# Optimization experiments

Measured on AMD Instinct MI355X. Metric: run time of the kernel, lower is better.

The kernel has to match this reference:

```python
import jax, jax.numpy as jnp
import numpy as np

EMBED_DIM = 1024
NUM_HEADS = 16
HEAD_DIM = EMBED_DIM // NUM_HEADS


def setup_inputs() -> dict:
    key = jax.random.key(0)
    ks = jax.random.split(key, 11)
    N, S, D = 2, 2048, EMBED_DIM
    scale = 1.0 / np.sqrt(D)
    inp = {
        "query": jax.random.normal(ks[0], (N, S, D), jnp.float32),
        "key": jax.random.normal(ks[1], (N, S, D), jnp.float32),
        "value": jax.random.normal(ks[2], (N, S, D), jnp.float32),
        # Dense layer params (kernel [D_in, D_out], bias [D_out])
        "Wq": jax.random.normal(ks[3], (D, D), jnp.float32) * scale,
        "bq": jnp.zeros((D,), jnp.float32),
        "Wk": jax.random.normal(ks[4], (D, D), jnp.float32) * scale,
        "bk": jnp.zeros((D,), jnp.float32),
        "Wv": jax.random.normal(ks[5], (D, D), jnp.float32) * scale,
        "bv": jnp.zeros((D,), jnp.float32),
        "Wp": jax.random.normal(ks[6], (D, D), jnp.float32) * scale,
        "bp": jnp.zeros((D,), jnp.float32),
    }
    return inp


def reference(query, key, value, Wq, bq, Wk, bk, Wv, bv, Wp, bp):
    N, S, D = query.shape
    H, Hd = NUM_HEADS, D // NUM_HEADS
    # Linear projections, then split heads: [N, H, S, Hd]
    def split_heads(x):
        return x.reshape(N, S, H, Hd).transpose(0, 2, 1, 3)
    q = split_heads(query @ Wq + bq)
    k = split_heads(key @ Wk + bk)
    v = split_heads(value @ Wv + bv)
    # Scaled dot-product attention; materializes [N, H, S, S] scores
    e = jnp.einsum("bhsd,bhtd->bhst", q, k) / jnp.sqrt(jnp.asarray(Hd, jnp.float32))
    a = jax.nn.softmax(e, axis=-1)
    # Dropout is identity in inference mode (keras Dropout default)
    out = jnp.einsum("bhst,bhtd->bhsd", a, v)
    out = out.transpose(0, 2, 1, 3).reshape(N, S, D)
    return out @ Wp + bp
```

## Files before the change

kernel.cpp:

```cpp
#include <hip/hip_runtime.h>
#include <cstdint>
#include <cstddef>

typedef _Float16 f16;
typedef f16 f16x2 __attribute__((ext_vector_type(2)));
typedef f16 f16x8 __attribute__((ext_vector_type(8)));
typedef __fp16 hf16x2 __attribute__((ext_vector_type(2)));
typedef float f32x4 __attribute__((ext_vector_type(4)));
typedef float f32x16 __attribute__((ext_vector_type(16)));
typedef unsigned int u32;

#define S_LEN 2048
#define DIM 1024
#define NBATCH 2
#define NHEAD 16
#define HDIM 64
#define M_TOT (NBATCH * S_LEN)

#define QSCALE 0.18033688011112042f

#define OFF_XQ 0ull
#define OFF_XK (OFF_XQ + (size_t)M_TOT * DIM * 2)
#define OFF_XV (OFF_XK + (size_t)M_TOT * DIM * 2)
#define OFF_WT (OFF_XV + (size_t)M_TOT * DIM * 2)
#define OFF_Q  (OFF_WT + 4ull * DIM * DIM * 2)
#define OFF_K  (OFF_Q + (size_t)M_TOT * DIM * 2)
#define OFF_VT (OFF_K + (size_t)M_TOT * DIM * 2)
#define OFF_AO (OFF_VT + (size_t)M_TOT * DIM * 2)

typedef const __attribute__((address_space(1))) void GVp;
typedef __attribute__((address_space(3))) void LVp;
__device__ __forceinline__ void gload16(const void* g, void* l) {
  __builtin_amdgcn_global_load_lds((GVp*)g, (LVp*)l, 16, 0, 0);
}

__device__ __forceinline__ float fast_exp2(float x) {
  float r;
  asm("v_exp_f32 %0, %1" : "=v"(r) : "v"(x));
  return r;
}

__global__ __launch_bounds__(256) void cast_x_kernel(
    const float* __restrict__ q, const float* __restrict__ k, const float* __restrict__ v,
    f16* __restrict__ oq, f16* __restrict__ ok, f16* __restrict__ ov) {
  const float* src = blockIdx.y == 0 ? q : blockIdx.y == 1 ? k : v;
  f16* dst = blockIdx.y == 0 ? oq : blockIdx.y == 1 ? ok : ov;
  size_t i = ((size_t)blockIdx.x * 256 + threadIdx.x) * 8;
  float4 a = *(const float4*)(src + i);
  float4 b = *(const float4*)(src + i + 4);
  f16x8 o;
  o[0] = (f16)a.x; o[1] = (f16)a.y; o[2] = (f16)a.z; o[3] = (f16)a.w;
  o[4] = (f16)b.x; o[5] = (f16)b.y; o[6] = (f16)b.z; o[7] = (f16)b.w;
  *(f16x8*)(dst + i) = o;
}

__global__ __launch_bounds__(256) void transpose_w_kernel(
    const float* __restrict__ Wq, const float* __restrict__ Wk,
    const float* __restrict__ Wv, const float* __restrict__ Wp,
    f16* __restrict__ out) {
  const float* W = blockIdx.z == 0 ? Wq : blockIdx.z == 1 ? Wk : blockIdx.z == 2 ? Wv : Wp;
  f16* Wt = out + (size_t)blockIdx.z * DIM * DIM;
  __shared__ f16 tile[64][72];
  const int kt = blockIdx.x * 64, nt = blockIdx.y * 64;
  const int t = threadIdx.x, r = t >> 2, c0 = (t & 3) * 16;
#pragma unroll
  for (int i = 0; i < 16; i += 4) {
    float4 vv = *(const float4*)(W + (size_t)(kt + r) * DIM + nt + c0 + i);
    tile[r][c0 + i + 0] = (f16)vv.x; tile[r][c0 + i + 1] = (f16)vv.y;
    tile[r][c0 + i + 2] = (f16)vv.z; tile[r][c0 + i + 3] = (f16)vv.w;
  }
  __syncthreads();
  f16x8 o0, o1;
#pragma unroll
  for (int i = 0; i < 8; ++i) { o0[i] = tile[c0 + i][r]; o1[i] = tile[c0 + 8 + i][r]; }
  *(f16x8*)(Wt + (size_t)(nt + r) * DIM + kt + c0) = o0;
  *(f16x8*)(Wt + (size_t)(nt + r) * DIM + kt + c0 + 8) = o1;
}

__device__ __forceinline__ void gemm_core(const f16* __restrict__ A, const f16* __restrict__ B,
                                          char* lds, f32x4 acc[4][4]) {
  const int tid = threadIdx.x;
  const int wid = tid >> 6, lane = tid & 63;
  const int l15 = lane & 15, l4 = lane >> 4;
  const int wm = (wid >> 1) * 64, wn = (wid & 1) * 64;
  const int srow = tid >> 2;
  const int scol = (tid & 3) * 8;
  const f16* gA = A + (size_t)srow * DIM + scol;
  const f16* gB = B + (size_t)srow * DIM + scol;
  const int ldst = wid * 1024;

  gload16(gA,            lds + ldst);
  gload16(gA + 64 * DIM, lds + 4096 + ldst);
  gload16(gB,            lds + 8192 + ldst);
  gload16(gB + 64 * DIM, lds + 12288 + ldst);
  __syncthreads();

  for (int kt = 0; kt < DIM / 32; ++kt) {
    char* cur = lds + (kt & 1) * 16384;
    if (kt + 1 < DIM / 32) {
      char* nxt = lds + ((kt + 1) & 1) * 16384;
      const f16* ga = gA + (kt + 1) * 32;
      const f16* gb = gB + (kt + 1) * 32;
      gload16(ga,            nxt + ldst);
      gload16(ga + 64 * DIM, nxt + 4096 + ldst);
      gload16(gb,            nxt + 8192 + ldst);
      gload16(gb + 64 * DIM, nxt + 12288 + ldst);
    }
    f16x8 af[4], bf[4];
#pragma unroll
    for (int mt = 0; mt < 4; ++mt)
      af[mt] = *(const f16x8*)(cur + (wm + mt * 16 + l15) * 64 + l4 * 16);
#pragma unroll
    for (int nt = 0; nt < 4; ++nt)
      bf[nt] = *(const f16x8*)(cur + 8192 + (wn + nt * 16 + l15) * 64 + l4 * 16);
#pragma unroll
    for (int mt = 0; mt < 4; ++mt)
#pragma unroll
      for (int nt = 0; nt < 4; ++nt)
        acc[mt][nt] = __builtin_amdgcn_mfma_f32_16x16x32_f16(af[mt], bf[nt], acc[mt][nt], 0, 0, 0);
    __syncthreads();
  }
}


__global__ __launch_bounds__(256) void proj_kernel(
    const f16* __restrict__ Xq, const f16* __restrict__ Xk, const f16* __restrict__ Xv,
    const f16* __restrict__ Wt,
    const float* __restrict__ bq, const float* __restrict__ bk, const float* __restrict__ bv,
    f16* __restrict__ Q, f16* __restrict__ Kh, f16* __restrict__ Vt) {
  __shared__ __align__(16) char lds[32768];
  const int m0 = blockIdx.x * 128, n0 = blockIdx.y * 128;
  const int z = blockIdx.z;
  const f16* X = z == 0 ? Xq : z == 1 ? Xk : Xv;
  const f16* W = Wt + (size_t)z * DIM * DIM;
  const float* bias = z == 0 ? bq : z == 1 ? bk : bv;
  f32x4 acc[4][4] = {};
  gemm_core(X + (size_t)m0 * DIM, W + (size_t)n0 * DIM, lds, acc);

  const int tid = threadIdx.x, wid = tid >> 6, lane = tid & 63;
  const int l15 = lane & 15, l4 = lane >> 4;
  const int wm = (wid >> 1) * 64, wn = (wid & 1) * 64;
#pragma unroll
  for (int nt = 0; nt < 4; ++nt) {
    const int col = n0 + wn + nt * 16 + l15;
    const float bb = bias[col];
    const int hh = col >> 6, d = col & 63;
#pragma unroll
    for (int mt = 0; mt < 4; ++mt)
#pragma unroll
      for (int j = 0; j < 4; ++j) {
        const int row = m0 + wm + mt * 16 + l4 * 4 + j;
        const float v = acc[mt][nt][j] + bb;
        const int n = row >> 11, s = row & (S_LEN - 1);
        const size_t panel = (size_t)(n * NHEAD + hh);
        if (z == 0) {
          const size_t a = panel * (S_LEN * HDIM) + (size_t)(s >> 5) * 2048 +
                           (d >> 4) * 512 + ((d >> 3) & 1) * 256 + (s & 31) * 8 + (d & 7);
          Q[a] = (f16)(v * QSCALE);
        } else if (z == 1) {
          const size_t a = panel * (S_LEN * HDIM) + (size_t)(s >> 5) * 2048 +
                           (d >> 4) * 512 + ((d >> 3) & 1) * 256 + (s & 31) * 8 + (d & 7);
          Kh[a] = (f16)v;
        } else {
          const size_t a = panel * (S_LEN * HDIM) + (size_t)(s >> 6) * 4096 +
                           (d >> 5) * 2048 + ((s >> 4) & 3) * 512 + ((s >> 3) & 1) * 256 +
                           (d & 31) * 8 + (s & 7);
          Vt[a] = (f16)v;
        }
      }
  }
}

__global__ __launch_bounds__(256) void outproj_kernel(
    const f16* __restrict__ A, const f16* __restrict__ Wt,
    const float* __restrict__ bias, float* __restrict__ Out) {
  __shared__ __align__(16) char lds[32768];
  const int m0 = blockIdx.x * 128, n0 = blockIdx.y * 128;
  f32x4 acc[4][4] = {};
  gemm_core(A + (size_t)m0 * DIM, Wt + (size_t)n0 * DIM, lds, acc);

  const int tid = threadIdx.x, wid = tid >> 6, lane = tid & 63;
  const int l15 = lane & 15, l4 = lane >> 4;
  const int wm = (wid >> 1) * 64, wn = (wid & 1) * 64;
#pragma unroll
  for (int nt = 0; nt < 4; ++nt) {
    const int col = n0 + wn + nt * 16 + l15;
    const float bb = bias[col];
#pragma unroll
    for (int mt = 0; mt < 4; ++mt)
#pragma unroll
      for (int j = 0; j < 4; ++j) {
        const int row = m0 + wm + mt * 16 + l4 * 4 + j;
        Out[(size_t)row * DIM + col] = acc[mt][nt][j] + bb;
      }
  }
}

__global__ __launch_bounds__(256, 2) void attn_kernel(
    const f16* __restrict__ Q, const f16* __restrict__ K,
    const f16* __restrict__ Vt, f16* __restrict__ AO) {
  const int qt = blockIdx.x, h = blockIdx.y, b = blockIdx.z;
  const int tid = threadIdx.x;
  const int lane = tid & 63, wid = tid >> 6;
  const int l31 = lane & 31, hi = lane >> 5;

  __shared__ __align__(16) char kv_lds[2][16384];

  const int q0 = qt * 128 + wid * 32;
  const size_t panel = (size_t)(b * NHEAD + h) * (S_LEN * HDIM);
  const f16* Qp = Q + panel + (size_t)(q0 >> 5) * 2048;
  const char* KpB = (const char*)(K + panel);
  const char* VpB = (const char*)(Vt + panel);

  f16x8 qf[4];
#pragma unroll
  for (int sk = 0; sk < 4; ++sk)
    qf[sk] = *(const f16x8*)(Qp + sk * 512 + hi * 256 + l31 * 8);

  f32x16 accO[2] = {};
  float lacc0 = 0.f, lacc1 = 0.f, lacc2 = 0.f, lacc3 = 0.f;

  auto STAGE = [&](int it, int buf) {
    const char* gK = KpB + (size_t)it * 8192 + tid * 16;
    const char* gV = VpB + (size_t)it * 8192 + tid * 16;
    char* lb = kv_lds[buf] + (tid >> 6) * 1024;
    gload16(gK,        lb);
    gload16(gK + 4096, lb + 4096);
    gload16(gV,        lb + 8192);
    gload16(gV + 4096, lb + 12288);
  };

  auto QK = [&](int buf, f32x16 (&st)[2]) {
    const char* lk = kv_lds[buf];
    f16x8 kf[2][4];
#pragma unroll
    for (int tt = 0; tt < 2; ++tt)
#pragma unroll
      for (int sk = 0; sk < 4; ++sk)
        kf[tt][sk] = *(const f16x8*)(lk + tt * 4096 + sk * 1024 + lane * 16);
    __builtin_amdgcn_s_setprio(1);
#pragma unroll
    for (int tt = 0; tt < 2; ++tt) {
      st[tt] = (f32x16)(0.f);
#pragma unroll
      for (int sk = 0; sk < 4; ++sk)
        st[tt] = __builtin_amdgcn_mfma_f32_32x32x16_f16(kf[tt][sk], qf[sk], st[tt], 0, 0, 0);
    }
    __builtin_amdgcn_s_setprio(0);
  };

  auto PHASE = [&](f32x16 (&st)[2], int buf) {
    const char* lv = kv_lds[buf] + 8192;
    f16x8 vf[2][4];
#pragma unroll
    for (int dt = 0; dt < 2; ++dt)
#pragma unroll
      for (int s = 0; s < 4; ++s)
        vf[dt][s] = *(const f16x8*)(lv + dt * 4096 + s * 1024 + lane * 16);

    u32 pk[2][8];
#pragma unroll
    for (int tt = 0; tt < 2; ++tt)
#pragma unroll
      for (int j = 0; j < 8; ++j) {
        const float p0 = fast_exp2(st[tt][2 * j]);
        const float p1 = fast_exp2(st[tt][2 * j + 1]);
        const float ps = p0 + p1;
        if (((tt * 8 + j) & 3) == 0) lacc0 += ps;
        else if (((tt * 8 + j) & 3) == 1) lacc1 += ps;
        else if (((tt * 8 + j) & 3) == 2) lacc2 += ps;
        else lacc3 += ps;
        union { hf16x2 h; u32 w; } cv;
        cv.h = __builtin_amdgcn_cvt_pkrtz(p0, p1);
        pk[tt][j] = cv.w;
      }

    __builtin_amdgcn_s_setprio(1);
#pragma unroll
    for (int s = 0; s < 4; ++s) {
      const int tt = s >> 1, sl = s & 1;
      u32 w0 = pk[tt][4 * sl + 0], w2 = pk[tt][4 * sl + 2];
      u32 w1 = pk[tt][4 * sl + 1], w3 = pk[tt][4 * sl + 3];
      asm("v_permlane32_swap_b32 %0, %1" : "+v"(w0), "+v"(w2));
      asm("v_permlane32_swap_b32 %0, %1" : "+v"(w1), "+v"(w3));
      union { u32 w[4]; f16x8 v; } pf;
      pf.w[0] = w0; pf.w[1] = w1; pf.w[2] = w2; pf.w[3] = w3;
      accO[0] = __builtin_amdgcn_mfma_f32_32x32x16_f16(vf[0][s], pf.v, accO[0], 0, 0, 0);
      accO[1] = __builtin_amdgcn_mfma_f32_32x32x16_f16(vf[1][s], pf.v, accO[1], 0, 0, 0);
    }
    __builtin_amdgcn_s_setprio(0);
  };

  const int NIT = S_LEN / 64;
  STAGE(0, 0);
  __syncthreads();

  f32x16 st[2];
  for (int it = 0; it < NIT; ++it) {
    const int buf = it & 1;
    if (it + 1 < NIT) STAGE(it + 1, buf ^ 1);
    QK(buf, st);
    PHASE(st, buf);
    __syncthreads();
  }

  const float l_loc = (lacc0 + lacc1) + (lacc2 + lacc3);
  const float l_all = l_loc + __shfl_xor(l_loc, 32);
  const float inv = 1.f / l_all;
  f16* aop = AO + ((size_t)(b * S_LEN + q0 + l31)) * DIM + h * HDIM;
#pragma unroll
  for (int dt = 0; dt < 2; ++dt)
#pragma unroll
    for (int j = 0; j < 8; ++j) {
      union { f16x2 h; u32 w; } cv;
      cv.h[0] = (f16)(accO[dt][2 * j] * inv);
      cv.h[1] = (f16)(accO[dt][2 * j + 1] * inv);
      const int d = ((2 * j) & 3) + 8 * ((2 * j) >> 2) + 4 * hi + dt * 32;
      *(f16x2*)(aop + d) = cv.h;
    }
}

extern "C" void kernel_launch(void* const* d_in, const int* in_sizes, int n_in,
                              void* d_out, int out_size, void* d_ws, size_t ws_size,
                              hipStream_t stream) {
  (void)in_sizes; (void)n_in; (void)out_size; (void)ws_size;
  const float* q  = (const float*)d_in[0];
  const float* k  = (const float*)d_in[1];
  const float* v  = (const float*)d_in[2];
  const float* Wq = (const float*)d_in[3];
  const float* bq = (const float*)d_in[4];
  const float* Wk = (const float*)d_in[5];
  const float* bk = (const float*)d_in[6];
  const float* Wv = (const float*)d_in[7];
  const float* bv = (const float*)d_in[8];
  const float* Wp = (const float*)d_in[9];
  const float* bp = (const float*)d_in[10];

  char* ws = (char*)d_ws;
  f16* Xq  = (f16*)(ws + OFF_XQ);
  f16* Xk  = (f16*)(ws + OFF_XK);
  f16* Xv  = (f16*)(ws + OFF_XV);
  f16* Wt  = (f16*)(ws + OFF_WT);
  f16* Qs  = (f16*)(ws + OFF_Q);
  f16* Kh  = (f16*)(ws + OFF_K);
  f16* Vts = (f16*)(ws + OFF_VT);
  f16* AO  = (f16*)(ws + OFF_AO);

  cast_x_kernel<<<dim3(2048, 3, 1), 256, 0, stream>>>(q, k, v, Xq, Xk, Xv);
  transpose_w_kernel<<<dim3(16, 16, 4), 256, 0, stream>>>(Wq, Wk, Wv, Wp, Wt);
  proj_kernel<<<dim3(32, 8, 3), 256, 0, stream>>>(Xq, Xk, Xv, Wt, bq, bk, bv, Qs, Kh, Vts);
  attn_kernel<<<dim3(16, 16, 2), 256, 0, stream>>>(Qs, Kh, Vts, AO);
  outproj_kernel<<<dim3(32, 8, 1), 256, 0, stream>>>(AO, Wt + 3ull * DIM * DIM, bp, (float*)d_out);
}
```

Measured before the change: 131.8 us.

## Split attention KV sequence across two wave groups and merge via LDS

The attention block grows to 512 threads, and two groups of four waves each handle half of the key/value sequence for the same 128 query rows. The partial outputs and row sums are then combined through shared memory before normalisation. This doubles the waves working on each query tile, which is meant to hide latency and keep the same grid of 512 blocks fuller on the GPU. The cost is a larger LDS footprint, an extra barrier and LDS round trip in the epilogue, and launch bounds of one block per 512 threads. Skipping the running max is safe because the combine is a plain sum.

```diff
diff --git a/kernel.cpp b/kernel.cpp
--- a/kernel.cpp
+++ b/kernel.cpp
@@ -196,17 +196,18 @@
   }
 }
 
-__global__ __launch_bounds__(256, 2) void attn_kernel(
+__global__ __launch_bounds__(512, 1) void attn_kernel(
     const f16* __restrict__ Q, const f16* __restrict__ K,
     const f16* __restrict__ Vt, f16* __restrict__ AO) {
   const int qt = blockIdx.x, h = blockIdx.y, b = blockIdx.z;
   const int tid = threadIdx.x;
   const int lane = tid & 63, wid = tid >> 6;
+  const int half = wid >> 2, widh = wid & 3;
   const int l31 = lane & 31, hi = lane >> 5;
 
-  __shared__ __align__(16) char kv_lds[2][16384];
-
-  const int q0 = qt * 128 + wid * 32;
+  __shared__ __align__(16) char kv_lds[2][2][16384];
+
+  const int q0 = qt * 128 + widh * 32;
   const size_t panel = (size_t)(b * NHEAD + h) * (S_LEN * HDIM);
   const f16* Qp = Q + panel + (size_t)(q0 >> 5) * 2048;
   const char* KpB = (const char*)(K + panel);
@@ -220,10 +221,13 @@
   f32x16 accO[2] = {};
   float lacc0 = 0.f, lacc1 = 0.f, lacc2 = 0.f, lacc3 = 0.f;
 
+  const int NIT = S_LEN / 64 / 2;
+
   auto STAGE = [&](int it, int buf) {
-    const char* gK = KpB + (size_t)it * 8192 + tid * 16;
-    const char* gV = VpB + (size_t)it * 8192 + tid * 16;
-    char* lb = kv_lds[buf] + (tid >> 6) * 1024;
+    const int gt = half * NIT + it;
+    const char* gK = KpB + (size_t)gt * 8192 + (widh * 64 + lane) * 16;
+    const char* gV = VpB + (size_t)gt * 8192 + (widh * 64 + lane) * 16;
+    char* lb = &kv_lds[half][buf][widh * 1024];
     gload16(gK,        lb);
     gload16(gK + 4096, lb + 4096);
     gload16(gV,        lb + 8192);
@@ -231,7 +235,7 @@
   };
 
   auto QK = [&](int buf, f32x16 (&st)[2]) {
-    const char* lk = kv_lds[buf];
+    const char* lk = &kv_lds[half][buf][0];
     f16x8 kf[2][4];
 #pragma unroll
     for (int tt = 0; tt < 2; ++tt)
@@ -250,7 +254,7 @@
   };
 
   auto PHASE = [&](f32x16 (&st)[2], int buf) {
-    const char* lv = kv_lds[buf] + 8192;
+    const char* lv = &kv_lds[half][buf][8192];
     f16x8 vf[2][4];
 #pragma unroll
     for (int dt = 0; dt < 2; ++dt)
@@ -291,7 +295,6 @@
     __builtin_amdgcn_s_setprio(0);
   };
 
-  const int NIT = S_LEN / 64;
   STAGE(0, 0);
   __syncthreads();
 
@@ -305,19 +308,39 @@
   }
 
   const float l_loc = (lacc0 + lacc1) + (lacc2 + lacc3);
-  const float l_all = l_loc + __shfl_xor(l_loc, 32);
-  const float inv = 1.f / l_all;
-  f16* aop = AO + ((size_t)(b * S_LEN + q0 + l31)) * DIM + h * HDIM;
-#pragma unroll
-  for (int dt = 0; dt < 2; ++dt)
-#pragma unroll
-    for (int j = 0; j < 8; ++j) {
-      union { f16x2 h; u32 w; } cv;
-      cv.h[0] = (f16)(accO[dt][2 * j] * inv);
-      cv.h[1] = (f16)(accO[dt][2 * j + 1] * inv);
-      const int d = ((2 * j) & 3) + 8 * ((2 * j) >> 2) + 4 * hi + dt * 32;
-      *(f16x2*)(aop + d) = cv.h;
-    }
+  float* comb = (float*)&kv_lds[0][0][0];
+  if (wid >= 4) {
+    float* base = comb + widh * 2048;
+#pragma unroll
+    for (int dt = 0; dt < 2; ++dt)
+#pragma unroll
+      for (int j = 0; j < 16; ++j)
+        base[(dt * 16 + j) * 64 + lane] = accO[dt][j];
+    comb[8192 + widh * 64 + lane] = l_loc;
+  }
+  __syncthreads();
+  if (wid < 4) {
+    float* base = comb + widh * 2048;
+#pragma unroll
+    for (int dt = 0; dt < 2; ++dt)
+#pragma unroll
+      for (int j = 0; j < 16; ++j)
+        accO[dt][j] += base[(dt * 16 + j) * 64 + lane];
+    const float l2 = l_loc + comb[8192 + widh * 64 + lane];
+    const float l_all = l2 + __shfl_xor(l2, 32);
+    const float inv = 1.f / l_all;
+    f16* aop = AO + ((size_t)(b * S_LEN + q0 + l31)) * DIM + h * HDIM;
+#pragma unroll
+    for (int dt = 0; dt < 2; ++dt)
+#pragma unroll
+      for (int j = 0; j < 8; ++j) {
+        union { f16x2 h; u32 w; } cv;
+        cv.h[0] = (f16)(accO[dt][2 * j] * inv);
+        cv.h[1] = (f16)(accO[dt][2 * j + 1] * inv);
+        const int d = ((2 * j) & 3) + 8 * ((2 * j) >> 2) + 4 * hi + dt * 32;
+        *(f16x2*)(aop + d) = cv.h;
+      }
+  }
 }
 
 extern "C" void kernel_launch(void* const* d_in, const int* in_sizes, int n_in,
@@ -349,6 +372,6 @@
   cast_x_kernel<<<dim3(2048, 3, 1), 256, 0, stream>>>(q, k, v, Xq, Xk, Xv);
   transpose_w_kernel<<<dim3(16, 16, 4), 256, 0, stream>>>(Wq, Wk, Wv, Wp, Wt);
   proj_kernel<<<dim3(32, 8, 3), 256, 0, stream>>>(Xq, Xk, Xv, Wt, bq, bk, bv, Qs, Kh, Vts);
-  attn_kernel<<<dim3(16, 16, 2), 256, 0, stream>>>(Qs, Kh, Vts, AO);
+  attn_kernel<<<dim3(16, 16, 2), 512, 0, stream>>>(Qs, Kh, Vts, AO);
   outproj_kernel<<<dim3(32, 8, 1), 256, 0, stream>>>(AO, Wt + 3ull * DIM * DIM, bp, (float*)d_out);
 }
```

Measured after the change: 134.6 us. +2.1%, slower.

## Triple-buffer K/V LDS staging with prefetch distance two in attention

Applied to the files above, without the earlier changes.

The attention loop now uses three LDS buffers instead of two and issues the K/V loads two tiles ahead. The full __syncthreads is replaced by an explicit vmcnt wait plus s_barrier, so only the oldest pending stage must land before compute. The goal is to hide more global-to-LDS latency behind the QK and PV MFMAs. The cost is 48KB of LDS per block instead of 32KB, which may limit occupancy, plus reliance on hand-counted vmcnt values.

```diff
diff --git a/kernel.cpp b/kernel.cpp
--- a/kernel.cpp
+++ b/kernel.cpp
@@ -204,7 +204,7 @@
   const int lane = tid & 63, wid = tid >> 6;
   const int l31 = lane & 31, hi = lane >> 5;
 
-  __shared__ __align__(16) char kv_lds[2][16384];
+  __shared__ __align__(16) char kv_lds[3][16384];
 
   const int q0 = qt * 128 + wid * 32;
   const size_t panel = (size_t)(b * NHEAD + h) * (S_LEN * HDIM);
@@ -223,7 +223,7 @@
   auto STAGE = [&](int it, int buf) {
     const char* gK = KpB + (size_t)it * 8192 + tid * 16;
     const char* gV = VpB + (size_t)it * 8192 + tid * 16;
-    char* lb = kv_lds[buf] + (tid >> 6) * 1024;
+    char* lb = &kv_lds[buf][wid * 1024];
     gload16(gK,        lb);
     gload16(gK + 4096, lb + 4096);
     gload16(gV,        lb + 8192);
@@ -231,7 +231,7 @@
   };
 
   auto QK = [&](int buf, f32x16 (&st)[2]) {
-    const char* lk = kv_lds[buf];
+    const char* lk = &kv_lds[buf][0];
     f16x8 kf[2][4];
 #pragma unroll
     for (int tt = 0; tt < 2; ++tt)
@@ -250,7 +250,7 @@
   };
 
   auto PHASE = [&](f32x16 (&st)[2], int buf) {
-    const char* lv = kv_lds[buf] + 8192;
+    const char* lv = &kv_lds[buf][8192];
     f16x8 vf[2][4];
 #pragma unroll
     for (int dt = 0; dt < 2; ++dt)
@@ -292,17 +292,31 @@
   };
 
   const int NIT = S_LEN / 64;
+
   STAGE(0, 0);
-  __syncthreads();
+  STAGE(1, 1);
 
   f32x16 st[2];
-  for (int it = 0; it < NIT; ++it) {
-    const int buf = it & 1;
-    if (it + 1 < NIT) STAGE(it + 1, buf ^ 1);
-    QK(buf, st);
-    PHASE(st, buf);
-    __syncthreads();
-  }
+  int bcur = 0;
+  for (int it = 0; it < NIT - 1; ++it) {
+    asm volatile("s_waitcnt vmcnt(4)" ::: "memory");
+    __builtin_amdgcn_sched_barrier(0);
+    __builtin_amdgcn_s_barrier();
+    __builtin_amdgcn_sched_barrier(0);
+    if (it + 2 < NIT) {
+      int bn = bcur + 2; if (bn >= 3) bn -= 3;
+      STAGE(it + 2, bn);
+    }
+    QK(bcur, st);
+    PHASE(st, bcur);
+    if (++bcur >= 3) bcur = 0;
+  }
+  asm volatile("s_waitcnt vmcnt(0)" ::: "memory");
+  __builtin_amdgcn_sched_barrier(0);
+  __builtin_amdgcn_s_barrier();
+  __builtin_amdgcn_sched_barrier(0);
+  QK(bcur, st);
+  PHASE(st, bcur);
 
   const float l_loc = (lacc0 + lacc1) + (lacc2 + lacc3);
   const float l_all = l_loc + __shfl_xor(l_loc, 32);
```

New measurement: 132.0 us. About the same (+0.1%).

## Split attention KV range across two blocks, add combine kernel, swizzle GEMM LDS

Applied to the files above, without the earlier changes.

Each attention block now handles only half of the key/value sequence. The grid doubles to 1024 blocks, and the launch bound asks for 4 blocks per CU to improve occupancy. Unnormalized partial outputs and row sums go to workspace (reusing the Xq/Xv cast buffers), and a new combine kernel sums them and normalizes. This works without a max correction because the softmax has no max subtraction. The projection GEMM core also gets an XOR swizzle on LDS columns to reduce bank conflicts. In exchange, the extra kernel launch and the fp16 partial round-trip add memory traffic and some rounding.

```diff
diff --git a/kernel.cpp b/kernel.cpp
--- a/kernel.cpp
+++ b/kernel.cpp
@@ -77,16 +77,16 @@
   *(f16x8*)(Wt + (size_t)(nt + r) * DIM + kt + c0 + 8) = o1;
 }
 
-__device__ __forceinline__ void gemm_core(const f16* __restrict__ A, const f16* __restrict__ B,
-                                          char* lds, f32x4 acc[4][4]) {
+__device__ __forceinline__ void gemm_core_sw(const f16* __restrict__ A, const f16* __restrict__ B,
+                                             char* lds, f32x4 acc[4][4]) {
   const int tid = threadIdx.x;
   const int wid = tid >> 6, lane = tid & 63;
   const int l15 = lane & 15, l4 = lane >> 4;
   const int wm = (wid >> 1) * 64, wn = (wid & 1) * 64;
-  const int srow = tid >> 2;
-  const int scol = (tid & 3) * 8;
-  const f16* gA = A + (size_t)srow * DIM + scol;
-  const f16* gB = B + (size_t)srow * DIM + scol;
+  const int rr = tid >> 2, cc = tid & 3;
+  const int ccs = cc ^ ((rr >> 1) & 3);
+  const f16* gA = A + (size_t)rr * DIM + ccs * 8;
+  const f16* gB = B + (size_t)rr * DIM + ccs * 8;
   const int ldst = wid * 1024;
 
   gload16(gA,            lds + ldst);
@@ -95,6 +95,7 @@
   gload16(gB + 64 * DIM, lds + 12288 + ldst);
   __syncthreads();
 
+  const int sw = (l15 >> 1) & 3;
   for (int kt = 0; kt < DIM / 32; ++kt) {
     char* cur = lds + (kt & 1) * 16384;
     if (kt + 1 < DIM / 32) {
@@ -109,10 +110,10 @@
     f16x8 af[4], bf[4];
 #pragma unroll
     for (int mt = 0; mt < 4; ++mt)
-      af[mt] = *(const f16x8*)(cur + (wm + mt * 16 + l15) * 64 + l4 * 16);
+      af[mt] = *(const f16x8*)(cur + (wm + mt * 16 + l15) * 64 + (l4 ^ sw) * 16);
 #pragma unroll
     for (int nt = 0; nt < 4; ++nt)
-      bf[nt] = *(const f16x8*)(cur + 8192 + (wn + nt * 16 + l15) * 64 + l4 * 16);
+      bf[nt] = *(const f16x8*)(cur + 8192 + (wn + nt * 16 + l15) * 64 + (l4 ^ sw) * 16);
 #pragma unroll
     for (int mt = 0; mt < 4; ++mt)
 #pragma unroll
@@ -135,7 +136,7 @@
   const f16* W = Wt + (size_t)z * DIM * DIM;
   const float* bias = z == 0 ? bq : z == 1 ? bk : bv;
   f32x4 acc[4][4] = {};
-  gemm_core(X + (size_t)m0 * DIM, W + (size_t)n0 * DIM, lds, acc);
+  gemm_core_sw(X + (size_t)m0 * DIM, W + (size_t)n0 * DIM, lds, acc);
 
   const int tid = threadIdx.x, wid = tid >> 6, lane = tid & 63;
   const int l15 = lane & 15, l4 = lane >> 4;
@@ -177,7 +178,7 @@
   __shared__ __align__(16) char lds[32768];
   const int m0 = blockIdx.x * 128, n0 = blockIdx.y * 128;
   f32x4 acc[4][4] = {};
-  gemm_core(A + (size_t)m0 * DIM, Wt + (size_t)n0 * DIM, lds, acc);
+  gemm_core_sw(A + (size_t)m0 * DIM, Wt + (size_t)n0 * DIM, lds, acc);
 
   const int tid = threadIdx.x, wid = tid >> 6, lane = tid & 63;
   const int l15 = lane & 15, l4 = lane >> 4;
@@ -196,10 +197,11 @@
   }
 }
 
-__global__ __launch_bounds__(256, 2) void attn_kernel(
+__global__ __launch_bounds__(256, 4) void attn_kernel(
     const f16* __restrict__ Q, const f16* __restrict__ K,
-    const f16* __restrict__ Vt, f16* __restrict__ AO) {
-  const int qt = blockIdx.x, h = blockIdx.y, b = blockIdx.z;
+    const f16* __restrict__ Vt, f16* __restrict__ partO, float* __restrict__ partL) {
+  const int qt = blockIdx.x, h = blockIdx.y;
+  const int b = blockIdx.z >> 1, half = blockIdx.z & 1;
   const int tid = threadIdx.x;
   const int lane = tid & 63, wid = tid >> 6;
   const int l31 = lane & 31, hi = lane >> 5;
@@ -220,10 +222,13 @@
   f32x16 accO[2] = {};
   float lacc0 = 0.f, lacc1 = 0.f, lacc2 = 0.f, lacc3 = 0.f;
 
+  const int NIT = 16;
+
   auto STAGE = [&](int it, int buf) {
-    const char* gK = KpB + (size_t)it * 8192 + tid * 16;
-    const char* gV = VpB + (size_t)it * 8192 + tid * 16;
-    char* lb = kv_lds[buf] + (tid >> 6) * 1024;
+    const size_t gt = (size_t)(half * NIT + it) * 8192;
+    const char* gK = KpB + gt + tid * 16;
+    const char* gV = VpB + gt + tid * 16;
+    char* lb = &kv_lds[buf][wid * 1024];
     gload16(gK,        lb);
     gload16(gK + 4096, lb + 4096);
     gload16(gV,        lb + 8192);
@@ -231,7 +236,7 @@
   };
 
   auto QK = [&](int buf, f32x16 (&st)[2]) {
-    const char* lk = kv_lds[buf];
+    const char* lk = &kv_lds[buf][0];
     f16x8 kf[2][4];
 #pragma unroll
     for (int tt = 0; tt < 2; ++tt)
@@ -250,7 +255,7 @@
   };
 
   auto PHASE = [&](f32x16 (&st)[2], int buf) {
-    const char* lv = kv_lds[buf] + 8192;
+    const char* lv = &kv_lds[buf][8192];
     f16x8 vf[2][4];
 #pragma unroll
     for (int dt = 0; dt < 2; ++dt)
@@ -291,7 +296,6 @@
     __builtin_amdgcn_s_setprio(0);
   };
 
-  const int NIT = S_LEN / 64;
   STAGE(0, 0);
   __syncthreads();
 
@@ -306,18 +310,40 @@
 
   const float l_loc = (lacc0 + lacc1) + (lacc2 + lacc3);
   const float l_all = l_loc + __shfl_xor(l_loc, 32);
-  const float inv = 1.f / l_all;
-  f16* aop = AO + ((size_t)(b * S_LEN + q0 + l31)) * DIM + h * HDIM;
+  const size_t pb = (((size_t)(half * NBATCH + b) * NHEAD + h) * S_LEN + q0 + l31) * HDIM;
 #pragma unroll
   for (int dt = 0; dt < 2; ++dt)
 #pragma unroll
     for (int j = 0; j < 8; ++j) {
       union { f16x2 h; u32 w; } cv;
-      cv.h[0] = (f16)(accO[dt][2 * j] * inv);
-      cv.h[1] = (f16)(accO[dt][2 * j + 1] * inv);
+      cv.h[0] = (f16)accO[dt][2 * j];
+      cv.h[1] = (f16)accO[dt][2 * j + 1];
       const int d = ((2 * j) & 3) + 8 * ((2 * j) >> 2) + 4 * hi + dt * 32;
-      *(f16x2*)(aop + d) = cv.h;
+      *(f16x2*)(partO + pb + d) = cv.h;
     }
+  if (hi == 0)
+    partL[((size_t)(half * NBATCH + b) * NHEAD + h) * S_LEN + q0 + l31] = l_all;
+}
+
+__global__ __launch_bounds__(256) void combine_kernel(
+    const f16* __restrict__ partO, const float* __restrict__ partL, f16* __restrict__ AO) {
+  const size_t idx = (size_t)blockIdx.x * 256 + threadIdx.x;
+  const size_t e = idx * 8;
+  const int d0 = (int)(e & 63);
+  const int q  = (int)((e >> 6) & (S_LEN - 1));
+  const int h  = (int)((e >> 17) & (NHEAD - 1));
+  const int b  = (int)(e >> 21);
+  const size_t base = (((size_t)b * NHEAD + h) * S_LEN + q) * HDIM + d0;
+  const size_t off1 = (size_t)NBATCH * NHEAD * S_LEN * HDIM;
+  f16x8 a0 = *(const f16x8*)(partO + base);
+  f16x8 a1 = *(const f16x8*)(partO + off1 + base);
+  const size_t lb = ((size_t)b * NHEAD + h) * S_LEN + q;
+  const float inv = 1.f / (partL[lb] + partL[(size_t)NBATCH * NHEAD * S_LEN + lb]);
+  f16x8 o;
+#pragma unroll
+  for (int i = 0; i < 8; ++i)
+    o[i] = (f16)(((float)a0[i] + (float)a1[i]) * inv);
+  *(f16x8*)(AO + ((size_t)(b * S_LEN + q)) * DIM + h * HDIM + d0) = o;
 }
 
 extern "C" void kernel_launch(void* const* d_in, const int* in_sizes, int n_in,
@@ -345,10 +371,13 @@
   f16* Kh  = (f16*)(ws + OFF_K);
   f16* Vts = (f16*)(ws + OFF_VT);
   f16* AO  = (f16*)(ws + OFF_AO);
+  f16* partO = (f16*)(ws + OFF_XQ);
+  float* partL = (float*)(ws + OFF_XV);
 
   cast_x_kernel<<<dim3(2048, 3, 1), 256, 0, stream>>>(q, k, v, Xq, Xk, Xv);
   transpose_w_kernel<<<dim3(16, 16, 4), 256, 0, stream>>>(Wq, Wk, Wv, Wp, Wt);
   proj_kernel<<<dim3(32, 8, 3), 256, 0, stream>>>(Xq, Xk, Xv, Wt, bq, bk, bv, Qs, Kh, Vts);
-  attn_kernel<<<dim3(16, 16, 2), 256, 0, stream>>>(Qs, Kh, Vts, AO);
+  attn_kernel<<<dim3(16, 16, 4), 256, 0, stream>>>(Qs, Kh, Vts, partO, partL);
+  combine_kernel<<<dim3(2048, 1, 1), 256, 0, stream>>>(partO, partL, AO);
   outproj_kernel<<<dim3(32, 8, 1), 256, 0, stream>>>(AO, Wt + 3ull * DIM * DIM, bp, (float*)d_out);
 }
```

New measurement: 140.5 us. 1.07x slower.
